# Optimization experiments

Hardware: AMD Instinct MI355X
Metric: run time of the kernel (lower is better)

The kernel has to match this reference:

```python
import jax, jax.numpy as jnp
import numpy as np

B, T, HID = 1, 2048, 4096
H, KVH, D = 32, 8, 128
N_REP = H // KVH
SCALE = D ** -0.5
EPS = 1e-6
THETA = 10000.0
TOPK, SINK, WIN = 256, 16, 256


def _rms_norm(x, w):
    var = jnp.mean(x * x, axis=-1, keepdims=True)
    return w * (x * jax.lax.rsqrt(var + EPS))


def _rotate_half(x):
    x1, x2 = x[..., : D // 2], x[..., D // 2 :]
    return jnp.concatenate([-x2, x1], axis=-1)


def setup_inputs() -> dict:
    key = jax.random.key(0)
    ks = jax.random.split(key, 6)
    hidden_states = jax.random.normal(ks[0], (B, T, HID), jnp.float32)
    Wq = jax.random.normal(ks[1], (HID, H * D), jnp.float32) * 0.02
    Wkv = jax.random.normal(ks[2], (HID, KVH * D), jnp.float32) * 0.02
    Wo = jax.random.normal(ks[3], (H * D, HID), jnp.float32) * 0.02
    q_norm_w = jnp.ones((D,), jnp.float32)
    k_norm_w = jnp.ones((D,), jnp.float32)
    # standard RoPE tables, theta=10000
    inv_freq = 1.0 / (THETA ** (jnp.arange(0, D, 2, dtype=jnp.float32) / D))
    freqs = jnp.arange(T, dtype=jnp.float32)[:, None] * inv_freq[None, :]  # (T, D/2)
    emb = jnp.concatenate([freqs, freqs], axis=-1)  # (T, D)
    cos = jnp.cos(emb)[None]  # (1, T, D)
    sin = jnp.sin(emb)[None]
    return {"hidden_states": hidden_states, "Wq": Wq, "Wkv": Wkv, "Wo": Wo,
            "q_norm_w": q_norm_w, "k_norm_w": k_norm_w, "cos": cos, "sin": sin}


def reference(hidden_states, Wq, Wkv, Wo, q_norm_w, k_norm_w, cos, sin):
    b, t, _ = hidden_states.shape
    s = t
    # projections -> (b, h, t, d)
    q = (hidden_states @ Wq).reshape(b, t, H, D).transpose(0, 2, 1, 3)
    kv = (hidden_states @ Wkv).reshape(b, t, KVH, D).transpose(0, 2, 1, 3)
    # qk RMSNorm per head_dim
    q = _rms_norm(q, q_norm_w)
    k = _rms_norm(kv, k_norm_w)
    v = kv  # latent KV: value shares the latent projection (no norm / rope)
    # rotary, cos/sin unsqueezed at head dim
    c = cos[:, None]  # (1,1,T,D)
    sn = sin[:, None]
    q = q * c + _rotate_half(q) * sn
    k = k * c + _rotate_half(k) * sn
    # GQA expansion
    k = jnp.repeat(k, N_REP, axis=1)
    v = jnp.repeat(v, N_REP, axis=1)
    # dense scores (reference path)
    scores = jnp.einsum("bhtd,bhsd->bhts", q, k) * SCALE  # (b,h,t,s)
    # ---- sparse DSA mask: sink | local window | per-query top-k, then causal ----
    q_idx = jnp.arange(t)
    k_idx = jnp.arange(s)
    sink = (k_idx < SINK)[None, None, None, :]
    local = (jnp.abs(q_idx[:, None] - k_idx[None, :]) <= WIN)[None, None]
    kth = jax.lax.top_k(scores, TOPK)[0][..., -1:]  # k-th largest per query
    topk_keep = scores >= kth
    causal_ok = (k_idx[None, :] <= q_idx[:, None])[None, None]
    keep = (sink | local | topk_keep) & causal_ok
    scores = jnp.where(keep, scores, -jnp.inf)
    attn = jax.nn.softmax(scores, axis=-1)
    out = jnp.einsum("bhts,bhsd->bhtd", attn, v)
    out = out.transpose(0, 2, 1, 3).reshape(b, t, H * D)
    return out @ Wo
```

## Files before the change

### kernel.cpp

```cpp
#include <hip/hip_runtime.h>
#include <hip/hip_bf16.h>

#define H 32
#define KVH 8
#define D 128
#define T 2048
#define HID 4096
#define TOPK 256
#define SINK 16
#define WIN 256
#define SCALE2 0.12753102600893415f
#define NPROJ 5120

#define SWZ(row, b) ((b) ^ (((row) & 7) << 4))

#define AS3(p) ((__attribute__((address_space(3))) void*)(p))
#define AS1(p) ((const __attribute__((address_space(1))) void*)(p))

typedef __attribute__((ext_vector_type(4))) float f32x4;
typedef __attribute__((ext_vector_type(8))) short short8;

__device__ __forceinline__ unsigned short f2bf(float f) {
  unsigned int b = __float_as_uint(f);
  b += 0x7FFFu + ((b >> 16) & 1u);
  return (unsigned short)(b >> 16);
}
__device__ __forceinline__ float bf2f(unsigned short u) {
  return __uint_as_float(((unsigned int)u) << 16);
}
__device__ __forceinline__ float ldf(const void* p, long i, bool b16) {
  return b16 ? bf2f(((const unsigned short*)p)[i]) : ((const float*)p)[i];
}
__device__ __forceinline__ bool bf16_mode(const unsigned int* probe) {
  return *probe == 0x3F803F80u;
}

__global__ void cvt_kernel(const void* __restrict__ src, unsigned short* __restrict__ dst,
                           long n, const unsigned int* probe) {
  bool b16 = bf16_mode(probe);
  long stride = (long)gridDim.x * blockDim.x;
  for (long i = (long)blockIdx.x * blockDim.x + threadIdx.x; i * 8 < n; i += stride) {
    long o = i * 8;
    if (b16) {
      *(uint4*)(dst + o) = *(const uint4*)((const unsigned short*)src + o);
    } else {
      const float* s = (const float*)src + o;
      float4 f0 = *(const float4*)s;
      float4 f1 = *(const float4*)(s + 4);
      uint4 v;
      v.x = (unsigned int)f2bf(f0.x) | ((unsigned int)f2bf(f0.y) << 16);
      v.y = (unsigned int)f2bf(f0.z) | ((unsigned int)f2bf(f0.w) << 16);
      v.z = (unsigned int)f2bf(f1.x) | ((unsigned int)f2bf(f1.y) << 16);
      v.w = (unsigned int)f2bf(f1.z) | ((unsigned int)f2bf(f1.w) << 16);
      *(uint4*)(dst + o) = v;
    }
  }
}

__global__ __launch_bounds__(256) void cvt_t(const void* __restrict__ src,
    unsigned short* __restrict__ dst, int R, int Cc, const unsigned int* probe) {
  __shared__ float tile[64][65];
  bool b16 = bf16_mode(probe);
  int r0 = blockIdx.y * 64, c0 = blockIdx.x * 64;
  int tid = threadIdx.x;
  int tr = tid >> 3;
  int tc8 = (tid & 7) * 8;
#pragma unroll
  for (int p = 0; p < 2; ++p) {
    int row = tr + p * 32;
    if (b16) {
      const unsigned short* s = (const unsigned short*)src + (size_t)(r0 + row) * Cc + c0 + tc8;
      uint4 d = *(const uint4*)s;
      const unsigned short* dv = (const unsigned short*)&d;
#pragma unroll
      for (int j = 0; j < 8; ++j) tile[row][tc8 + j] = bf2f(dv[j]);
    } else {
      const float* s = (const float*)src + (size_t)(r0 + row) * Cc + c0 + tc8;
      float4 f0 = *(const float4*)s;
      float4 f1 = *(const float4*)(s + 4);
      tile[row][tc8 + 0] = f0.x; tile[row][tc8 + 1] = f0.y;
      tile[row][tc8 + 2] = f0.z; tile[row][tc8 + 3] = f0.w;
      tile[row][tc8 + 4] = f1.x; tile[row][tc8 + 5] = f1.y;
      tile[row][tc8 + 6] = f1.z; tile[row][tc8 + 7] = f1.w;
    }
  }
  __syncthreads();
#pragma unroll
  for (int p = 0; p < 2; ++p) {
    int oc = tr + p * 32;
    unsigned short tmp[8];
#pragma unroll
    for (int j = 0; j < 8; ++j) tmp[j] = f2bf(tile[tc8 + j][oc]);
    *(uint4*)(dst + (size_t)(c0 + oc) * R + r0 + tc8) = *(uint4*)tmp;
  }
}

__global__ __launch_bounds__(256) void gemm_bf16(
    const unsigned short* __restrict__ A, const unsigned short* __restrict__ Bt,
    void* __restrict__ C, int M, int N, int K, const unsigned int* probe, int outmode) {
  __shared__ alignas(16) unsigned short As[128 * 32];
  __shared__ alignas(16) unsigned short Bs[128 * 32];
  int lin = blockIdx.x;
  int qq = (int)gridDim.x >> 3;
  int swz = (lin & 7) * qq + (lin >> 3);
  int nx = N >> 7;
  int n0 = (swz % nx) * 128, m0 = (swz / nx) * 128;
  int tid = threadIdx.x;
  int w = tid >> 6, l = tid & 63;
  int wm = (w >> 1) * 64, wn = (w & 1) * 64;
  int lr = l & 15, lg = l >> 4;

  int srow0 = (w * 2 + 0) * 16 + (l >> 2);
  int srow1 = (w * 2 + 1) * 16 + (l >> 2);
  int cch = l & 3;
  int sf0 = (srow0 ^ (srow0 >> 2)) & 3;
  int sf1 = (srow1 ^ (srow1 >> 2)) & 3;
  const unsigned short* gA0 = A + (size_t)(m0 + srow0) * K + ((cch ^ sf0) * 8);
  const unsigned short* gA1 = A + (size_t)(m0 + srow1) * K + ((cch ^ sf1) * 8);
  const unsigned short* gB0 = Bt + (size_t)(n0 + srow0) * K + ((cch ^ sf0) * 8);
  const unsigned short* gB1 = Bt + (size_t)(n0 + srow1) * K + ((cch ^ sf1) * 8);
  unsigned short* lA0 = As + (w * 2 + 0) * 16 * 32;
  unsigned short* lA1 = As + (w * 2 + 1) * 16 * 32;
  unsigned short* lB0 = Bs + (w * 2 + 0) * 16 * 32;
  unsigned short* lB1 = Bs + (w * 2 + 1) * 16 * 32;

  const unsigned short* pa[4];
  const unsigned short* pb[4];
#pragma unroll
  for (int i = 0; i < 4; ++i) {
    int ra = wm + i * 16 + lr;
    int fa = (ra ^ (ra >> 2)) & 3;
    pa[i] = As + ra * 32 + ((lg ^ fa) * 8);
    int rb = wn + i * 16 + lr;
    int fb = (rb ^ (rb >> 2)) & 3;
    pb[i] = Bs + rb * 32 + ((lg ^ fb) * 8);
  }

  f32x4 zero = {0.f, 0.f, 0.f, 0.f};
  f32x4 acc[4][4];
#pragma unroll
  for (int i = 0; i < 4; ++i)
#pragma unroll
    for (int j = 0; j < 4; ++j) acc[i][j] = zero;

  for (int k0 = 0; k0 < K; k0 += 32) {
    __builtin_amdgcn_global_load_lds(AS1(gA0 + k0), AS3(lA0), 16, 0, 0);
    __builtin_amdgcn_global_load_lds(AS1(gA1 + k0), AS3(lA1), 16, 0, 0);
    __builtin_amdgcn_global_load_lds(AS1(gB0 + k0), AS3(lB0), 16, 0, 0);
    __builtin_amdgcn_global_load_lds(AS1(gB1 + k0), AS3(lB1), 16, 0, 0);
    __syncthreads();
    short8 a[4], b[4];
#pragma unroll
    for (int i = 0; i < 4; ++i) {
      a[i] = *(const short8*)pa[i];
      b[i] = *(const short8*)pb[i];
    }
#pragma unroll
    for (int i = 0; i < 4; ++i)
#pragma unroll
      for (int j = 0; j < 4; ++j)
        acc[i][j] = __builtin_amdgcn_mfma_f32_16x16x32_bf16(a[i], b[j], acc[i][j], 0, 0, 0);
    __syncthreads();
  }
  bool b16out = (outmode == 1) || (outmode == 2 && bf16_mode(probe));
#pragma unroll
  for (int i = 0; i < 4; ++i)
#pragma unroll
    for (int j = 0; j < 4; ++j)
#pragma unroll
      for (int r = 0; r < 4; ++r) {
        int row = m0 + wm + i * 16 + lg * 4 + r;
        int col = n0 + wn + j * 16 + lr;
        float v = acc[i][j][r];
        if (b16out) ((unsigned short*)C)[(size_t)row * N + col] = f2bf(v);
        else ((float*)C)[(size_t)row * N + col] = v;
      }
}

__global__ __launch_bounds__(256) void qk_prep(
    const unsigned short* __restrict__ Proj, const void* nw, const void* cosp, const void* sinp,
    unsigned short* __restrict__ Qh, const unsigned int* probe) {
  bool b16 = bf16_mode(probe);
  int w = threadIdx.x >> 6, l = threadIdx.x & 63;
  int gw = blockIdx.x * 4 + w;
  int t = gw >> 5, h = gw & 31;
  const unsigned short* x = Proj + (size_t)t * NPROJ + h * D;
  float x1 = bf2f(x[l]), x2 = bf2f(x[l + 64]);
  float s = x1 * x1 + x2 * x2;
  for (int m = 32; m; m >>= 1) s += __shfl_xor(s, m);
  float inv = rsqrtf(s * (1.0f / D) + 1e-6f);
  float w1 = ldf(nw, l, b16), w2 = ldf(nw, l + 64, b16);
  float c1 = ldf(cosp, (long)t * D + l, b16), c2 = ldf(cosp, (long)t * D + l + 64, b16);
  float s1 = ldf(sinp, (long)t * D + l, b16), s2 = ldf(sinp, (long)t * D + l + 64, b16);
  float xn1 = x1 * inv * w1, xn2 = x2 * inv * w2;
  unsigned short* o = Qh + (size_t)h * T * D + (size_t)t * D;
  o[l] = f2bf(SCALE2 * (xn1 * c1 - xn2 * s1));
  o[l + 64] = f2bf(SCALE2 * (xn2 * c2 + xn1 * s2));
}

__global__ __launch_bounds__(256) void kv_prep(
    const unsigned short* __restrict__ Proj, const void* nw, const void* cosp, const void* sinp,
    unsigned short* __restrict__ Kh, unsigned short* __restrict__ Vt, const unsigned int* probe) {
  bool b16 = bf16_mode(probe);
  int w = threadIdx.x >> 6, l = threadIdx.x & 63;
  int gw = blockIdx.x * 4 + w;
  int t = gw >> 3, h = gw & 7;
  const unsigned short* x = Proj + (size_t)t * NPROJ + (H * D) + h * D;
  float x1 = bf2f(x[l]), x2 = bf2f(x[l + 64]);
  Vt[(size_t)h * D * T + (size_t)l * T + t] = x[l];
  Vt[(size_t)h * D * T + (size_t)(l + 64) * T + t] = x[l + 64];
  float s = x1 * x1 + x2 * x2;
  for (int m = 32; m; m >>= 1) s += __shfl_xor(s, m);
  float inv = rsqrtf(s * (1.0f / D) + 1e-6f);
  float w1 = ldf(nw, l, b16), w2 = ldf(nw, l + 64, b16);
  float c1 = ldf(cosp, (long)t * D + l, b16), c2 = ldf(cosp, (long)t * D + l + 64, b16);
  float s1 = ldf(sinp, (long)t * D + l, b16), s2 = ldf(sinp, (long)t * D + l + 64, b16);
  float xn1 = x1 * inv * w1, xn2 = x2 * inv * w2;
  unsigned short* o = Kh + (size_t)h * T * D + (size_t)t * D;
  o[l] = f2bf(xn1 * c1 - xn2 * s1);
  o[l + 64] = f2bf(xn2 * c2 + xn1 * s2);
}

__global__ __launch_bounds__(1024, 8) void attn_kernel(
    const unsigned short* __restrict__ Qh, const unsigned short* __restrict__ Kh,
    const unsigned short* __restrict__ Vt, unsigned short* __restrict__ attn_out) {
  __shared__ alignas(16) unsigned short sc[16][2048];
  __shared__ alignas(16) unsigned short qt[16 * 128];
  __shared__ alignas(16) float part[8][64][4];
  __shared__ float zinv[16];
  int t0 = blockIdx.x * 16;
  int h = blockIdx.y;
  int hk = h >> 2;
  int tid = threadIdx.x;
  int w = tid >> 6, l = tid & 63;
  int lr = l & 15, lg = l >> 4;
  f32x4 zero = {0.f, 0.f, 0.f, 0.f};
  char* scB = (char*)sc;

  {
    int row = tid >> 6;
    int bir = (tid & 63) * 4;
    const unsigned int* qsrc = (const unsigned int*)(Qh + (size_t)h * (T * D) + (size_t)t0 * D);
    *(unsigned int*)((char*)qt + row * 256 + SWZ(row, bir)) = qsrc[tid];
  }
  __syncthreads();

  {
    short8 aq[4];
#pragma unroll
    for (int kk = 0; kk < 4; ++kk)
      aq[kk] = *(const short8*)((const char*)qt + lr * 256 + SWZ(lr, kk * 64 + lg * 16));
    const unsigned short* Kb = Kh + (size_t)hk * (T * D) + (size_t)lr * D + lg * 8;
    short8 kf0, kf1, kf2, kf3;
    {
      const unsigned short* kp = Kb + (size_t)(w * 16) * D;
      kf0 = *(const short8*)(kp);
      kf1 = *(const short8*)(kp + 32);
      kf2 = *(const short8*)(kp + 64);
      kf3 = *(const short8*)(kp + 96);
    }
#pragma unroll
    for (int ii = 0; ii < 8; ++ii) {
      int st = w + ii * 16;
      int stn = (ii < 7) ? (st + 16) : st;
      const unsigned short* kp = Kb + (size_t)(stn * 16) * D;
      f32x4 acc = zero;
      acc = __builtin_amdgcn_mfma_f32_16x16x32_bf16(kf0, aq[0], acc, 0, 0, 0);
      kf0 = *(const short8*)(kp);
      acc = __builtin_amdgcn_mfma_f32_16x16x32_bf16(kf1, aq[1], acc, 0, 0, 0);
      kf1 = *(const short8*)(kp + 32);
      acc = __builtin_amdgcn_mfma_f32_16x16x32_bf16(kf2, aq[2], acc, 0, 0, 0);
      kf2 = *(const short8*)(kp + 64);
      acc = __builtin_amdgcn_mfma_f32_16x16x32_bf16(kf3, aq[3], acc, 0, 0, 0);
      kf3 = *(const short8*)(kp + 96);
      uint2 pk;
      pk.x = (unsigned int)f2bf(acc[0]) | ((unsigned int)f2bf(acc[1]) << 16);
      pk.y = (unsigned int)f2bf(acc[2]) | ((unsigned int)f2bf(acc[3]) << 16);
      *(uint2*)(scB + lr * 4096 + SWZ(lr, st * 32 + lg * 8)) = pk;
    }
  }
  __syncthreads();

  {
    int row = w, tq = t0 + row;
    int rsw = (row & 7) << 4;
    int lim = (t0 + 15) >> 7;
    char* rb = scB + row * 4096;
    unsigned int klo[16], khi[16];
#pragma unroll
    for (int i = 0; i < 16; ++i) {
      unsigned int b = *(const unsigned int*)(rb + ((256 * i + 4 * l) ^ rsw));
      unsigned int m = (b >> 15) & 0x00010001u;
      unsigned int kk2 = b ^ (0x80008000u | (m * 0x7FFFu));
      klo[i] = kk2 & 0xFFFFu;
      khi[i] = kk2 >> 16;
    }
    unsigned int um = 0;
#pragma unroll
    for (int i = 0; i < 16; ++i) {
      unsigned int a_ = klo[i] > khi[i] ? klo[i] : khi[i];
      um = um > a_ ? um : a_;
    }
    for (int m = 32; m; m >>= 1) {
      unsigned int o = (unsigned int)__shfl_xor((int)um, m);
      um = um > o ? um : o;
    }
    unsigned int lo = 0, hi = um;
    {
      unsigned int mid = um > 192u ? um - 192u : 1u;
      int cnt = 0;
#pragma unroll
      for (int i = 0; i < 16; ++i)
        cnt += (int)__popcll(__ballot(klo[i] >= mid)) + (int)__popcll(__ballot(khi[i] >= mid));
      if (cnt >= TOPK) lo = mid; else hi = mid - 1u;
    }
    if (lo == 0u && um > 1024u) {
      unsigned int mid = um - 1024u;
      int cnt = 0;
#pragma unroll
      for (int i = 0; i < 16; ++i)
        cnt += (int)__popcll(__ballot(klo[i] >= mid)) + (int)__popcll(__ballot(khi[i] >= mid));
      if (cnt >= TOPK) lo = mid; else hi = mid - 1u;
    }
    while (lo < hi) {
      unsigned int mid = (lo + hi + 1u) >> 1;
      int cnt = 0;
#pragma unroll
      for (int i = 0; i < 16; ++i)
        cnt += (int)__popcll(__ballot(klo[i] >= mid)) + (int)__popcll(__ballot(khi[i] >= mid));
      if (cnt >= TOPK) lo = mid; else hi = mid - 1u;
    }
    unsigned int thr = lo;

    int ca0 = (tq - 2 * l) >> 7;
    int ca1 = (tq - 2 * l - 1) >> 7;
    int wa0 = (tq - WIN - 2 * l + 127) >> 7;
    int wa1 = (tq - WIN - 2 * l - 1 + 127) >> 7;
    bool snk = (l < 8);
    unsigned int mA = 0, mB = 0, mk = 0;
#pragma unroll
    for (int i = 0; i < 16; ++i) {
      if (i > lim) break;
      bool k0 = (i <= ca0) && (((i == 0) && snk) || (i >= wa0) || (klo[i] >= thr));
      bool k1 = (i <= ca1) && (((i == 0) && snk) || (i >= wa1) || (khi[i] >= thr));
      if (k0) { mA |= (1u << i); mk = mk > klo[i] ? mk : klo[i]; }
      if (k1) { mB |= (1u << i); mk = mk > khi[i] ? mk : khi[i]; }
    }
    for (int m = 32; m; m >>= 1) {
      unsigned int o = (unsigned int)__shfl_xor((int)mk, m);
      mk = mk > o ? mk : o;
    }
    unsigned int mb = (mk & 0x8000u) ? (mk ^ 0x8000u) : ((~mk) & 0xFFFFu);
    float mx = bf2f((unsigned short)mb);

    float z = 0.f;
#pragma unroll
    for (int i = 0; i < 16; ++i) {
      if (i > lim) break;
      unsigned int b0 = (klo[i] & 0x8000u) ? (klo[i] ^ 0x8000u) : ((~klo[i]) & 0xFFFFu);
      unsigned int b1 = (khi[i] & 0x8000u) ? (khi[i] ^ 0x8000u) : ((~khi[i]) & 0xFFFFu);
      float x0 = bf2f((unsigned short)b0) - mx;
      float x1 = bf2f((unsigned short)b1) - mx;
      float e0x, e1x;
      asm("v_exp_f32 %0, %1" : "=v"(e0x) : "v"(x0));
      asm("v_exp_f32 %0, %1" : "=v"(e1x) : "v"(x1));
      float e0 = ((mA >> i) & 1u) ? e0x : 0.f;
      float e1 = ((mB >> i) & 1u) ? e1x : 0.f;
      z += e0 + e1;
      *(unsigned int*)(rb + ((256 * i + 4 * l) ^ rsw)) =
          (unsigned int)f2bf(e0) | ((unsigned int)f2bf(e1) << 16);
    }
    for (int m = 32; m; m >>= 1) z += __shfl_xor(z, m);
    if (l == 0) zinv[row] = 1.0f / z;
  }
  __syncthreads();

  {
    int half = w >> 3;
    int d0 = (w & 7) * 16;
    const unsigned short* Vb = Vt + (size_t)hk * (D * T) + (size_t)(d0 + lr) * T + lg * 8;
    const char* prb = scB + lr * 4096;
    int psw = (lr & 7) << 4;
    f32x4 o0 = zero, o1 = zero;
    int ks_end = (t0 + 47) >> 5;
    int ks_endE = (ks_end + 1) & ~1;
    int kmid = ((ks_endE >> 1) + 1) & ~1;
    int ksA = half ? kmid : 0;
    int ksB = half ? ks_endE : kmid;
    short8 vb0 = *(const short8*)(Vb + ksA * 32);
    short8 vb1 = *(const short8*)(Vb + (ksA + 1) * 32);
#pragma unroll 2
    for (int ks = ksA; ks < ksB; ks += 2) {
      int kn = (ks + 2 < ksB) ? (ks + 2) : ks;
      short8 pa0 = *(const short8*)(prb + ((ks * 64 + lg * 16) ^ psw));
      o0 = __builtin_amdgcn_mfma_f32_16x16x32_bf16(vb0, pa0, o0, 0, 0, 0);
      vb0 = *(const short8*)(Vb + kn * 32);
      short8 pa1 = *(const short8*)(prb + (((ks + 1) * 64 + lg * 16) ^ psw));
      o1 = __builtin_amdgcn_mfma_f32_16x16x32_bf16(vb1, pa1, o1, 0, 0, 0);
      vb1 = *(const short8*)(Vb + (kn + 1) * 32);
    }
    f32x4 oo;
#pragma unroll
    for (int r = 0; r < 4; ++r) oo[r] = o0[r] + o1[r];
    if (half) *(f32x4*)(&part[w & 7][l][0]) = oo;
    __syncthreads();
    if (!half) {
      f32x4 po = *(const f32x4*)(&part[w & 7][l][0]);
      float rz = zinv[lr];
      unsigned short tmp[4];
#pragma unroll
      for (int r = 0; r < 4; ++r) tmp[r] = f2bf((oo[r] + po[r]) * rz);
      unsigned short* dst = attn_out + (size_t)(t0 + lr) * (H * D) + h * D + d0 + lg * 4;
      *(uint2*)dst = *(uint2*)tmp;
    }
  }
}

extern "C" void kernel_launch(void* const* d_in, const int* in_sizes, int n_in,
                              void* d_out, int out_size, void* d_ws, size_t ws_size,
                              hipStream_t stream) {
  (void)in_sizes; (void)n_in; (void)out_size; (void)ws_size;
  const void* hs = d_in[0];
  const void* Wq = d_in[1];
  const void* Wkv = d_in[2];
  const void* Wo = d_in[3];
  const unsigned int* probe = (const unsigned int*)d_in[4];
  const void* knw = d_in[5];
  const void* cosp = d_in[6];
  const void* sinp = d_in[7];

  char* ws = (char*)d_ws;
  unsigned short* WqT_bf = (unsigned short*)(ws);
  unsigned short* WkvT_bf= (unsigned short*)(ws + 33554432);
  unsigned short* WoT_bf = (unsigned short*)(ws + 41943040);
  unsigned short* hid_bf = (unsigned short*)(ws + 75497472);
  unsigned short* Proj_bf= (unsigned short*)(ws + 92274688);
  unsigned short* Qh     = (unsigned short*)(ws + 134217728);
  unsigned short* Kh     = (unsigned short*)(ws + 150994944);
  unsigned short* Vt     = (unsigned short*)(ws + 155189248);
  unsigned short* attn_bf= (unsigned short*)(ws + 159383552);

  hipLaunchKernelGGL(cvt_kernel, dim3(1024), dim3(256), 0, stream, hs, hid_bf, (long)T * HID, probe);
  hipLaunchKernelGGL(cvt_t, dim3(64, 64), dim3(256), 0, stream, Wq, WqT_bf, HID, H * D, probe);
  hipLaunchKernelGGL(cvt_t, dim3(16, 64), dim3(256), 0, stream, Wkv, WkvT_bf, HID, KVH * D, probe);
  hipLaunchKernelGGL(cvt_t, dim3(64, 64), dim3(256), 0, stream, Wo, WoT_bf, H * D, HID, probe);

  hipLaunchKernelGGL(gemm_bf16, dim3(640), dim3(256), 0, stream,
                     hid_bf, WqT_bf, (void*)Proj_bf, 2048, NPROJ, 4096,
                     (const unsigned int*)nullptr, 1);

  hipLaunchKernelGGL(qk_prep, dim3(16384), dim3(256), 0, stream, Proj_bf, d_in[4], cosp, sinp, Qh, probe);
  hipLaunchKernelGGL(kv_prep, dim3(4096), dim3(256), 0, stream, Proj_bf, knw, cosp, sinp, Kh, Vt, probe);

  hipLaunchKernelGGL(attn_kernel, dim3(128, 32), dim3(1024), 0, stream, Qh, Kh, Vt, attn_bf);

  hipLaunchKernelGGL(gemm_bf16, dim3(512), dim3(256), 0, stream,
                     attn_bf, WoT_bf, d_out, 2048, 4096, 4096, probe, 2);
}
```

Measured before the change: 743.4 us.

## Split attention into a batched QK score GEMM and a separate sparse-softmax-PV kernel

```diff
diff --git a/kernel.cpp b/kernel.cpp
--- a/kernel.cpp
+++ b/kernel.cpp
@@ -174,6 +174,88 @@
         float v = acc[i][j][r];
         if (b16out) ((unsigned short*)C)[(size_t)row * N + col] = f2bf(v);
         else ((float*)C)[(size_t)row * N + col] = v;
+      }
+}
+
+__global__ __launch_bounds__(256) void gemm_qk(
+    const unsigned short* __restrict__ Qall, const unsigned short* __restrict__ Kall,
+    unsigned short* __restrict__ Sout) {
+  __shared__ alignas(16) unsigned short As[128 * 32];
+  __shared__ alignas(16) unsigned short Bs[128 * 32];
+  int lin = blockIdx.x;
+  int swz = (lin & 7) * 32 + (lin >> 3);
+  int n0 = (swz & 15) * 128, m0 = (swz >> 4) * 128;
+  int h = blockIdx.y;
+  const unsigned short* A = Qall + (size_t)h * (T * D);
+  const unsigned short* Bt = Kall + (size_t)(h >> 2) * (T * D);
+  unsigned short* C = Sout + (size_t)h * T * T;
+  int tid = threadIdx.x;
+  int w = tid >> 6, l = tid & 63;
+  int wm = (w >> 1) * 64, wn = (w & 1) * 64;
+  int lr = l & 15, lg = l >> 4;
+
+  int srow0 = (w * 2 + 0) * 16 + (l >> 2);
+  int srow1 = (w * 2 + 1) * 16 + (l >> 2);
+  int cch = l & 3;
+  int sf0 = (srow0 ^ (srow0 >> 2)) & 3;
+  int sf1 = (srow1 ^ (srow1 >> 2)) & 3;
+  const unsigned short* gA0 = A + (size_t)(m0 + srow0) * D + ((cch ^ sf0) * 8);
+  const unsigned short* gA1 = A + (size_t)(m0 + srow1) * D + ((cch ^ sf1) * 8);
+  const unsigned short* gB0 = Bt + (size_t)(n0 + srow0) * D + ((cch ^ sf0) * 8);
+  const unsigned short* gB1 = Bt + (size_t)(n0 + srow1) * D + ((cch ^ sf1) * 8);
+  unsigned short* lA0 = As + (w * 2 + 0) * 16 * 32;
+  unsigned short* lA1 = As + (w * 2 + 1) * 16 * 32;
+  unsigned short* lB0 = Bs + (w * 2 + 0) * 16 * 32;
+  unsigned short* lB1 = Bs + (w * 2 + 1) * 16 * 32;
+
+  const unsigned short* pa[4];
+  const unsigned short* pb[4];
+#pragma unroll
+  for (int i = 0; i < 4; ++i) {
+    int ra = wm + i * 16 + lr;
+    int fa = (ra ^ (ra >> 2)) & 3;
+    pa[i] = As + ra * 32 + ((lg ^ fa) * 8);
+    int rb = wn + i * 16 + lr;
+    int fb = (rb ^ (rb >> 2)) & 3;
+    pb[i] = Bs + rb * 32 + ((lg ^ fb) * 8);
+  }
+
+  f32x4 zero = {0.f, 0.f, 0.f, 0.f};
+  f32x4 acc[4][4];
+#pragma unroll
+  for (int i = 0; i < 4; ++i)
+#pragma unroll
+    for (int j = 0; j < 4; ++j) acc[i][j] = zero;
+
+#pragma unroll
+  for (int k0 = 0; k0 < D; k0 += 32) {
+    __builtin_amdgcn_global_load_lds(AS1(gA0 + k0), AS3(lA0), 16, 0, 0);
+    __builtin_amdgcn_global_load_lds(AS1(gA1 + k0), AS3(lA1), 16, 0, 0);
+    __builtin_amdgcn_global_load_lds(AS1(gB0 + k0), AS3(lB0), 16, 0, 0);
+    __builtin_amdgcn_global_load_lds(AS1(gB1 + k0), AS3(lB1), 16, 0, 0);
+    __syncthreads();
+    short8 a[4], b[4];
+#pragma unroll
+    for (int i = 0; i < 4; ++i) {
+      a[i] = *(const short8*)pa[i];
+      b[i] = *(const short8*)pb[i];
+    }
+#pragma unroll
+    for (int i = 0; i < 4; ++i)
+#pragma unroll
+      for (int j = 0; j < 4; ++j)
+        acc[i][j] = __builtin_amdgcn_mfma_f32_16x16x32_bf16(a[i], b[j], acc[i][j], 0, 0, 0);
+    __syncthreads();
+  }
+#pragma unroll
+  for (int i = 0; i < 4; ++i)
+#pragma unroll
+    for (int j = 0; j < 4; ++j)
+#pragma unroll
+      for (int r = 0; r < 4; ++r) {
+        int row = m0 + wm + i * 16 + lg * 4 + r;
+        int col = n0 + wn + j * 16 + lr;
+        C[(size_t)row * T + col] = f2bf(acc[i][j][r]);
       }
 }
 
@@ -219,6 +301,164 @@
   unsigned short* o = Kh + (size_t)h * T * D + (size_t)t * D;
   o[l] = f2bf(xn1 * c1 - xn2 * s1);
   o[l + 64] = f2bf(xn2 * c2 + xn1 * s2);
+}
+
+__global__ __launch_bounds__(1024, 8) void attn_sm(
+    const unsigned short* __restrict__ S,
+    const unsigned short* __restrict__ Vt, unsigned short* __restrict__ attn_out) {
+  __shared__ alignas(16) unsigned short sc[16][2048];
+  __shared__ alignas(16) float part[8][64][4];
+  __shared__ float zinv[16];
+  int t0 = blockIdx.x * 16;
+  int h = blockIdx.y;
+  int hk = h >> 2;
+  int tid = threadIdx.x;
+  int w = tid >> 6, l = tid & 63;
+  int lr = l & 15, lg = l >> 4;
+  f32x4 zero = {0.f, 0.f, 0.f, 0.f};
+  char* scB = (char*)sc;
+
+  {
+    int row = w, tq = t0 + row;
+    int rsw = (row & 7) << 4;
+    int lim = (t0 + 15) >> 7;
+    char* rb = scB + row * 4096;
+    const unsigned int* Sr = (const unsigned int*)(S + ((size_t)h * T + tq) * T);
+#pragma unroll
+    for (int i = 0; i < 16; ++i)
+      *(unsigned int*)(rb + ((256 * i + 4 * l) ^ rsw)) = Sr[l + 64 * i];
+    unsigned int klo[16], khi[16];
+#pragma unroll
+    for (int i = 0; i < 16; ++i) {
+      unsigned int b = *(const unsigned int*)(rb + ((256 * i + 4 * l) ^ rsw));
+      unsigned int m = (b >> 15) & 0x00010001u;
+      unsigned int kk2 = b ^ (0x80008000u | (m * 0x7FFFu));
+      klo[i] = kk2 & 0xFFFFu;
+      khi[i] = kk2 >> 16;
+    }
+    unsigned int um = 0;
+#pragma unroll
+    for (int i = 0; i < 16; ++i) {
+      unsigned int a_ = klo[i] > khi[i] ? klo[i] : khi[i];
+      um = um > a_ ? um : a_;
+    }
+    for (int m = 32; m; m >>= 1) {
+      unsigned int o = (unsigned int)__shfl_xor((int)um, m);
+      um = um > o ? um : o;
+    }
+    unsigned int lo = 0, hi = um;
+    {
+      unsigned int mid = um > 192u ? um - 192u : 1u;
+      int cnt = 0;
+#pragma unroll
+      for (int i = 0; i < 16; ++i)
+        cnt += (int)__popcll(__ballot(klo[i] >= mid)) + (int)__popcll(__ballot(khi[i] >= mid));
+      if (cnt >= TOPK) lo = mid; else hi = mid - 1u;
+    }
+    if (lo == 0u && um > 1024u) {
+      unsigned int mid = um - 1024u;
+      int cnt = 0;
+#pragma unroll
+      for (int i = 0; i < 16; ++i)
+        cnt += (int)__popcll(__ballot(klo[i] >= mid)) + (int)__popcll(__ballot(khi[i] >= mid));
+      if (cnt >= TOPK) lo = mid; else hi = mid - 1u;
+    }
+    while (lo < hi) {
+      unsigned int mid = (lo + hi + 1u) >> 1;
+      int cnt = 0;
+#pragma unroll
+      for (int i = 0; i < 16; ++i)
+        cnt += (int)__popcll(__ballot(klo[i] >= mid)) + (int)__popcll(__ballot(khi[i] >= mid));
+      if (cnt >= TOPK) lo = mid; else hi = mid - 1u;
+    }
+    unsigned int thr = lo;
+
+    int ca0 = (tq - 2 * l) >> 7;
+    int ca1 = (tq - 2 * l - 1) >> 7;
+    int wa0 = (tq - WIN - 2 * l + 127) >> 7;
+    int wa1 = (tq - WIN - 2 * l - 1 + 127) >> 7;
+    bool snk = (l < 8);
+    unsigned int mA = 0, mB = 0, mk = 0;
+#pragma unroll
+    for (int i = 0; i < 16; ++i) {
+      if (i > lim) break;
+      bool k0 = (i <= ca0) && (((i == 0) && snk) || (i >= wa0) || (klo[i] >= thr));
+      bool k1 = (i <= ca1) && (((i == 0) && snk) || (i >= wa1) || (khi[i] >= thr));
+      if (k0) { mA |= (1u << i); mk = mk > klo[i] ? mk : klo[i]; }
+      if (k1) { mB |= (1u << i); mk = mk > khi[i] ? mk : khi[i]; }
+    }
+    for (int m = 32; m; m >>= 1) {
+      unsigned int o = (unsigned int)__shfl_xor((int)mk, m);
+      mk = mk > o ? mk : o;
+    }
+    unsigned int mb = (mk & 0x8000u) ? (mk ^ 0x8000u) : ((~mk) & 0xFFFFu);
+    float mx = bf2f((unsigned short)mb);
+
+    float z = 0.f;
+#pragma unroll
+    for (int i = 0; i < 16; ++i) {
+      if (i > lim) break;
+      unsigned int b0 = (klo[i] & 0x8000u) ? (klo[i] ^ 0x8000u) : ((~klo[i]) & 0xFFFFu);
+      unsigned int b1 = (khi[i] & 0x8000u) ? (khi[i] ^ 0x8000u) : ((~khi[i]) & 0xFFFFu);
+      float x0 = bf2f((unsigned short)b0) - mx;
+      float x1 = bf2f((unsigned short)b1) - mx;
+      float e0x, e1x;
+      asm("v_exp_f32 %0, %1" : "=v"(e0x) : "v"(x0));
+      asm("v_exp_f32 %0, %1" : "=v"(e1x) : "v"(x1));
+      float e0 = ((mA >> i) & 1u) ? e0x : 0.f;
+      float e1 = ((mB >> i) & 1u) ? e1x : 0.f;
+      z += e0 + e1;
+      *(unsigned int*)(rb + ((256 * i + 4 * l) ^ rsw)) =
+          (unsigned int)f2bf(e0) | ((unsigned int)f2bf(e1) << 16);
+    }
+    for (int m = 32; m; m >>= 1) z += __shfl_xor(z, m);
+    if (l == 0) zinv[row] = 1.0f / z;
+  }
+  __syncthreads();
+
+  {
+    int half = w >> 3;
+    int d0 = (w & 7) * 16;
+    const unsigned short* Vb = Vt + (size_t)hk * (D * T) + (size_t)(d0 + lr) * T + lg * 8;
+    const char* prb = scB + lr * 4096;
+    int psw = (lr & 7) << 4;
+    f32x4 o0 = zero, o1 = zero;
+    int ks_end = (t0 + 47) >> 5;
+    int ks_endE = (ks_end + 1) & ~1;
+    int kmid = ((ks_endE >> 1) + 1) & ~1;
+    int ksA = half ? kmid : 0;
+    int ksB = half ? ks_endE : kmid;
+    short8 vb0 = *(const short8*)(Vb + ksA * 32);
+    short8 vb1 = *(const short8*)(Vb + (ksA + 1) * 32);
+#pragma unroll 2
+    for (int ks = ksA; ks < ksB; ks += 2) {
+      int kn = (ks + 2 < ksB) ? (ks + 2) : ks;
+      short8 pa0 = *(const short8*)(prb + ((ks * 64 + lg * 16) ^ psw));
+      __builtin_amdgcn_s_setprio(1);
+      o0 = __builtin_amdgcn_mfma_f32_16x16x32_bf16(vb0, pa0, o0, 0, 0, 0);
+      __builtin_amdgcn_s_setprio(0);
+      vb0 = *(const short8*)(Vb + kn * 32);
+      short8 pa1 = *(const short8*)(prb + (((ks + 1) * 64 + lg * 16) ^ psw));
+      __builtin_amdgcn_s_setprio(1);
+      o1 = __builtin_amdgcn_mfma_f32_16x16x32_bf16(vb1, pa1, o1, 0, 0, 0);
+      __builtin_amdgcn_s_setprio(0);
+      vb1 = *(const short8*)(Vb + (kn + 1) * 32);
+    }
+    f32x4 oo;
+#pragma unroll
+    for (int r = 0; r < 4; ++r) oo[r] = o0[r] + o1[r];
+    if (half) *(f32x4*)(&part[w & 7][l][0]) = oo;
+    __syncthreads();
+    if (!half) {
+      f32x4 po = *(const f32x4*)(&part[w & 7][l][0]);
+      float rz = zinv[lr];
+      unsigned short tmp[4];
+#pragma unroll
+      for (int r = 0; r < 4; ++r) tmp[r] = f2bf((oo[r] + po[r]) * rz);
+      unsigned short* dst = attn_out + (size_t)(t0 + lr) * (H * D) + h * D + d0 + lg * 4;
+      *(uint2*)dst = *(uint2*)tmp;
+    }
+  }
 }
 
 __global__ __launch_bounds__(1024, 8) void attn_kernel(
@@ -419,7 +659,7 @@
 extern "C" void kernel_launch(void* const* d_in, const int* in_sizes, int n_in,
                               void* d_out, int out_size, void* d_ws, size_t ws_size,
                               hipStream_t stream) {
-  (void)in_sizes; (void)n_in; (void)out_size; (void)ws_size;
+  (void)in_sizes; (void)n_in; (void)out_size;
   const void* hs = d_in[0];
   const void* Wq = d_in[1];
   const void* Wkv = d_in[2];
@@ -439,6 +679,8 @@
   unsigned short* Kh     = (unsigned short*)(ws + 150994944);
   unsigned short* Vt     = (unsigned short*)(ws + 155189248);
   unsigned short* attn_bf= (unsigned short*)(ws + 159383552);
+  const size_t S_off = 176160768;
+  const size_t S_bytes = (size_t)H * T * T * 2;
 
   hipLaunchKernelGGL(cvt_kernel, dim3(1024), dim3(256), 0, stream, hs, hid_bf, (long)T * HID, probe);
   hipLaunchKernelGGL(cvt_t, dim3(64, 64), dim3(256), 0, stream, Wq, WqT_bf, HID, H * D, probe);
@@ -452,7 +694,13 @@
   hipLaunchKernelGGL(qk_prep, dim3(16384), dim3(256), 0, stream, Proj_bf, d_in[4], cosp, sinp, Qh, probe);
   hipLaunchKernelGGL(kv_prep, dim3(4096), dim3(256), 0, stream, Proj_bf, knw, cosp, sinp, Kh, Vt, probe);
 
-  hipLaunchKernelGGL(attn_kernel, dim3(128, 32), dim3(1024), 0, stream, Qh, Kh, Vt, attn_bf);
+  if (ws_size >= S_off + S_bytes) {
+    unsigned short* S = (unsigned short*)(ws + S_off);
+    hipLaunchKernelGGL(gemm_qk, dim3(256, 32), dim3(256), 0, stream, Qh, Kh, S);
+    hipLaunchKernelGGL(attn_sm, dim3(128, 32), dim3(1024), 0, stream, S, Vt, attn_bf);
+  } else {
+    hipLaunchKernelGGL(attn_kernel, dim3(128, 32), dim3(1024), 0, stream, Qh, Kh, Vt, attn_bf);
+  }
 
   hipLaunchKernelGGL(gemm_bf16, dim3(512), dim3(256), 0, stream,
                      attn_bf, WoT_bf, d_out, 2048, 4096, 4096, probe, 2);
```

Result: no change. 743.3 us (-0.0%).

## Split QK scores into separate tiled GEMM staged through global scratch buffer

Applied to the files above, without the earlier changes.

```diff
diff --git a/kernel.cpp b/kernel.cpp
--- a/kernel.cpp
+++ b/kernel.cpp
@@ -174,6 +174,88 @@
         float v = acc[i][j][r];
         if (b16out) ((unsigned short*)C)[(size_t)row * N + col] = f2bf(v);
         else ((float*)C)[(size_t)row * N + col] = v;
+      }
+}
+
+__global__ __launch_bounds__(256) void gemm_qk(
+    const unsigned short* __restrict__ Qall, const unsigned short* __restrict__ Kall,
+    unsigned short* __restrict__ Sout, int h0) {
+  __shared__ alignas(16) unsigned short As[128 * 32];
+  __shared__ alignas(16) unsigned short Bs[128 * 32];
+  int lin = blockIdx.x;
+  int swz = (lin & 7) * 32 + (lin >> 3);
+  int n0 = (swz & 15) * 128, m0 = (swz >> 4) * 128;
+  int h = h0 + blockIdx.y;
+  const unsigned short* A = Qall + (size_t)h * (T * D);
+  const unsigned short* Bt = Kall + (size_t)(h >> 2) * (T * D);
+  unsigned short* C = Sout + (size_t)blockIdx.y * T * T;
+  int tid = threadIdx.x;
+  int w = tid >> 6, l = tid & 63;
+  int wm = (w >> 1) * 64, wn = (w & 1) * 64;
+  int lr = l & 15, lg = l >> 4;
+
+  int srow0 = (w * 2 + 0) * 16 + (l >> 2);
+  int srow1 = (w * 2 + 1) * 16 + (l >> 2);
+  int cch = l & 3;
+  int sf0 = (srow0 ^ (srow0 >> 2)) & 3;
+  int sf1 = (srow1 ^ (srow1 >> 2)) & 3;
+  const unsigned short* gA0 = A + (size_t)(m0 + srow0) * D + ((cch ^ sf0) * 8);
+  const unsigned short* gA1 = A + (size_t)(m0 + srow1) * D + ((cch ^ sf1) * 8);
+  const unsigned short* gB0 = Bt + (size_t)(n0 + srow0) * D + ((cch ^ sf0) * 8);
+  const unsigned short* gB1 = Bt + (size_t)(n0 + srow1) * D + ((cch ^ sf1) * 8);
+  unsigned short* lA0 = As + (w * 2 + 0) * 16 * 32;
+  unsigned short* lA1 = As + (w * 2 + 1) * 16 * 32;
+  unsigned short* lB0 = Bs + (w * 2 + 0) * 16 * 32;
+  unsigned short* lB1 = Bs + (w * 2 + 1) * 16 * 32;
+
+  const unsigned short* pa[4];
+  const unsigned short* pb[4];
+#pragma unroll
+  for (int i = 0; i < 4; ++i) {
+    int ra = wm + i * 16 + lr;
+    int fa = (ra ^ (ra >> 2)) & 3;
+    pa[i] = As + ra * 32 + ((lg ^ fa) * 8);
+    int rb = wn + i * 16 + lr;
+    int fb = (rb ^ (rb >> 2)) & 3;
+    pb[i] = Bs + rb * 32 + ((lg ^ fb) * 8);
+  }
+
+  f32x4 zero = {0.f, 0.f, 0.f, 0.f};
+  f32x4 acc[4][4];
+#pragma unroll
+  for (int i = 0; i < 4; ++i)
+#pragma unroll
+    for (int j = 0; j < 4; ++j) acc[i][j] = zero;
+
+#pragma unroll
+  for (int k0 = 0; k0 < D; k0 += 32) {
+    __builtin_amdgcn_global_load_lds(AS1(gA0 + k0), AS3(lA0), 16, 0, 0);
+    __builtin_amdgcn_global_load_lds(AS1(gA1 + k0), AS3(lA1), 16, 0, 0);
+    __builtin_amdgcn_global_load_lds(AS1(gB0 + k0), AS3(lB0), 16, 0, 0);
+    __builtin_amdgcn_global_load_lds(AS1(gB1 + k0), AS3(lB1), 16, 0, 0);
+    __syncthreads();
+    short8 a[4], b[4];
+#pragma unroll
+    for (int i = 0; i < 4; ++i) {
+      a[i] = *(const short8*)pa[i];
+      b[i] = *(const short8*)pb[i];
+    }
+#pragma unroll
+    for (int i = 0; i < 4; ++i)
+#pragma unroll
+      for (int j = 0; j < 4; ++j)
+        acc[i][j] = __builtin_amdgcn_mfma_f32_16x16x32_bf16(a[i], b[j], acc[i][j], 0, 0, 0);
+    __syncthreads();
+  }
+#pragma unroll
+  for (int i = 0; i < 4; ++i)
+#pragma unroll
+    for (int j = 0; j < 4; ++j)
+#pragma unroll
+      for (int r = 0; r < 4; ++r) {
+        int row = m0 + wm + i * 16 + lg * 4 + r;
+        int col = n0 + wn + j * 16 + lr;
+        C[(size_t)row * T + col] = f2bf(acc[i][j][r]);
       }
 }
 
@@ -221,15 +303,14 @@
   o[l + 64] = f2bf(xn2 * c2 + xn1 * s2);
 }
 
-__global__ __launch_bounds__(1024, 8) void attn_kernel(
-    const unsigned short* __restrict__ Qh, const unsigned short* __restrict__ Kh,
-    const unsigned short* __restrict__ Vt, unsigned short* __restrict__ attn_out) {
+__global__ __launch_bounds__(1024, 8) void attn_sm(
+    const unsigned short* __restrict__ S,
+    const unsigned short* __restrict__ Vt, unsigned short* __restrict__ attn_out, int h0) {
   __shared__ alignas(16) unsigned short sc[16][2048];
-  __shared__ alignas(16) unsigned short qt[16 * 128];
   __shared__ alignas(16) float part[8][64][4];
   __shared__ float zinv[16];
   int t0 = blockIdx.x * 16;
-  int h = blockIdx.y;
+  int h = h0 + blockIdx.y;
   int hk = h >> 2;
   int tid = threadIdx.x;
   int w = tid >> 6, l = tid & 63;
@@ -238,54 +319,14 @@
   char* scB = (char*)sc;
 
   {
-    int row = tid >> 6;
-    int bir = (tid & 63) * 4;
-    const unsigned int* qsrc = (const unsigned int*)(Qh + (size_t)h * (T * D) + (size_t)t0 * D);
-    *(unsigned int*)((char*)qt + row * 256 + SWZ(row, bir)) = qsrc[tid];
-  }
-  __syncthreads();
-
-  {
-    short8 aq[4];
-#pragma unroll
-    for (int kk = 0; kk < 4; ++kk)
-      aq[kk] = *(const short8*)((const char*)qt + lr * 256 + SWZ(lr, kk * 64 + lg * 16));
-    const unsigned short* Kb = Kh + (size_t)hk * (T * D) + (size_t)lr * D + lg * 8;
-    short8 kf0, kf1, kf2, kf3;
-    {
-      const unsigned short* kp = Kb + (size_t)(w * 16) * D;
-      kf0 = *(const short8*)(kp);
-      kf1 = *(const short8*)(kp + 32);
-      kf2 = *(const short8*)(kp + 64);
-      kf3 = *(const short8*)(kp + 96);
-    }
-#pragma unroll
-    for (int ii = 0; ii < 8; ++ii) {
-      int st = w + ii * 16;
-      int stn = (ii < 7) ? (st + 16) : st;
-      const unsigned short* kp = Kb + (size_t)(stn * 16) * D;
-      f32x4 acc = zero;
-      acc = __builtin_amdgcn_mfma_f32_16x16x32_bf16(kf0, aq[0], acc, 0, 0, 0);
-      kf0 = *(const short8*)(kp);
-      acc = __builtin_amdgcn_mfma_f32_16x16x32_bf16(kf1, aq[1], acc, 0, 0, 0);
-      kf1 = *(const short8*)(kp + 32);
-      acc = __builtin_amdgcn_mfma_f32_16x16x32_bf16(kf2, aq[2], acc, 0, 0, 0);
-      kf2 = *(const short8*)(kp + 64);
-      acc = __builtin_amdgcn_mfma_f32_16x16x32_bf16(kf3, aq[3], acc, 0, 0, 0);
-      kf3 = *(const short8*)(kp + 96);
-      uint2 pk;
-      pk.x = (unsigned int)f2bf(acc[0]) | ((unsigned int)f2bf(acc[1]) << 16);
-      pk.y = (unsigned int)f2bf(acc[2]) | ((unsigned int)f2bf(acc[3]) << 16);
-      *(uint2*)(scB + lr * 4096 + SWZ(lr, st * 32 + lg * 8)) = pk;
-    }
-  }
-  __syncthreads();
-
-  {
     int row = w, tq = t0 + row;
     int rsw = (row & 7) << 4;
     int lim = (t0 + 15) >> 7;
     char* rb = scB + row * 4096;
+    const unsigned int* Sr = (const unsigned int*)(S + ((size_t)blockIdx.y * T + tq) * T);
+#pragma unroll
+    for (int i = 0; i < 16; ++i)
+      *(unsigned int*)(rb + ((256 * i + 4 * l) ^ rsw)) = Sr[l + 64 * i];
     unsigned int klo[16], khi[16];
 #pragma unroll
     for (int i = 0; i < 16; ++i) {
@@ -393,10 +434,14 @@
     for (int ks = ksA; ks < ksB; ks += 2) {
       int kn = (ks + 2 < ksB) ? (ks + 2) : ks;
       short8 pa0 = *(const short8*)(prb + ((ks * 64 + lg * 16) ^ psw));
+      __builtin_amdgcn_s_setprio(1);
       o0 = __builtin_amdgcn_mfma_f32_16x16x32_bf16(vb0, pa0, o0, 0, 0, 0);
+      __builtin_amdgcn_s_setprio(0);
       vb0 = *(const short8*)(Vb + kn * 32);
       short8 pa1 = *(const short8*)(prb + (((ks + 1) * 64 + lg * 16) ^ psw));
+      __builtin_amdgcn_s_setprio(1);
       o1 = __builtin_amdgcn_mfma_f32_16x16x32_bf16(vb1, pa1, o1, 0, 0, 0);
+      __builtin_amdgcn_s_setprio(0);
       vb1 = *(const short8*)(Vb + (kn + 1) * 32);
     }
     f32x4 oo;
@@ -419,7 +464,7 @@
 extern "C" void kernel_launch(void* const* d_in, const int* in_sizes, int n_in,
                               void* d_out, int out_size, void* d_ws, size_t ws_size,
                               hipStream_t stream) {
-  (void)in_sizes; (void)n_in; (void)out_size; (void)ws_size;
+  (void)in_sizes; (void)n_in; (void)out_size;
   const void* hs = d_in[0];
   const void* Wq = d_in[1];
   const void* Wkv = d_in[2];
@@ -439,6 +484,8 @@
   unsigned short* Kh     = (unsigned short*)(ws + 150994944);
   unsigned short* Vt     = (unsigned short*)(ws + 155189248);
   unsigned short* attn_bf= (unsigned short*)(ws + 159383552);
+  const size_t S_off = 176160768;
+  const size_t HEAD_S = (size_t)T * T * 2;
 
   hipLaunchKernelGGL(cvt_kernel, dim3(1024), dim3(256), 0, stream, hs, hid_bf, (long)T * HID, probe);
   hipLaunchKernelGGL(cvt_t, dim3(64, 64), dim3(256), 0, stream, Wq, WqT_bf, HID, H * D, probe);
@@ -452,7 +499,21 @@
   hipLaunchKernelGGL(qk_prep, dim3(16384), dim3(256), 0, stream, Proj_bf, d_in[4], cosp, sinp, Qh, probe);
   hipLaunchKernelGGL(kv_prep, dim3(4096), dim3(256), 0, stream, Proj_bf, knw, cosp, sinp, Kh, Vt, probe);
 
-  hipLaunchKernelGGL(attn_kernel, dim3(128, 32), dim3(1024), 0, stream, Qh, Kh, Vt, attn_bf);
+  size_t tail = (ws_size > S_off) ? (ws_size - S_off) / HEAD_S : 0;
+  unsigned short* Sbuf;
+  int cap;
+  if (tail >= 6) {
+    Sbuf = (unsigned short*)(ws + S_off);
+    cap = (int)(tail < (size_t)H ? tail : (size_t)H);
+  } else {
+    Sbuf = (unsigned short*)ws;
+    cap = 5;
+  }
+  for (int h0 = 0; h0 < H; h0 += cap) {
+    int cnt = (H - h0 < cap) ? (H - h0) : cap;
+    hipLaunchKernelGGL(gemm_qk, dim3(256, cnt), dim3(256), 0, stream, Qh, Kh, Sbuf, h0);
+    hipLaunchKernelGGL(attn_sm, dim3(128, cnt), dim3(1024), 0, stream, Sbuf, Vt, attn_bf, h0);
+  }
 
   hipLaunchKernelGGL(gemm_bf16, dim3(512), dim3(256), 0, stream,
                      attn_bf, WoT_bf, d_out, 2048, 4096, 4096, probe, 2);
```

After: 722.3 us. -2.8%, faster.
